# Kernel tuning notes

Measured on AMD Instinct MI355X. Metric: run time of the kernel, lower is better.

Reference implementation:

```python
import jax, jax.numpy as jnp
import numpy as np

ALPHA = 0.2  # LeakyReLU negative slope


def setup_inputs() -> dict:
    key = jax.random.key(0)
    k1, k2, k3, k4 = jax.random.split(key, 4)
    N, Fin, Fout = 8192, 256, 64
    inputs = {
        "input": jax.random.normal(k1, (N, Fin), dtype=jnp.float32),
        "adj": jax.random.randint(k2, (N, N), 0, 2, dtype=jnp.int32),
        "W": jax.random.normal(k3, (Fin, Fout), dtype=jnp.float32) * (1.414 * np.sqrt(2.0 / (Fin + Fout))),
        "a": jax.random.normal(k4, (2 * Fout, 1), dtype=jnp.float32) * (1.414 * np.sqrt(2.0 / (2 * Fout + 1))),
    }
    return inputs


def reference(input, adj, W, a):
    # h: [N, Fout]
    h = input @ W
    Fout = h.shape[1]
    # Decompose pairwise score: e[i,j] = leakyrelu(h[i]@a1 + h[j]@a2)
    # (mathematically identical to the original concat+matmul construction,
    #  but avoids the O(N^2 * 2F) intermediate)
    a1, a2 = a[:Fout, 0], a[Fout:, 0]
    s1 = h @ a1  # [N]
    s2 = h @ a2  # [N]
    e = jax.nn.leaky_relu(s1[:, None] + s2[None, :], negative_slope=ALPHA)  # [N, N]
    # Mask non-edges with -10 (as in the original), row softmax
    masked = jnp.where(adj > 0, e, jnp.float32(-10.0))
    attention = jax.nn.softmax(masked, axis=1)
    # dropout p=0.0 (eval/reference mode): identity
    h_prime = attention @ h  # [N, Fout]
    return jax.nn.elu(h_prime)  # concat=True path
```

## Files before the change

### kernel.cpp

```cpp
#include <hip/hip_runtime.h>
#include <hip/hip_bf16.h>
#include <cstdint>
#include <cstddef>

#define NN 8192
#define FIN 256
#define FOUT 64
#define ALPHA_SLOPE 0.2f
#define EXP_M10 4.5399929762484854e-05f

#define JSPLIT 2
#define STRIP 128
#define NSTRIP ((NN / JSPLIT) / STRIP)
#define WPITCH 272
#define HPITCH 272
#define CP 68

typedef short s16x8 __attribute__((ext_vector_type(8)));
typedef float f32x4 __attribute__((ext_vector_type(4)));
typedef int   i32x4 __attribute__((ext_vector_type(4)));

__device__ __forceinline__ unsigned short f2bf(float x) {
    union { float f; uint32_t u; } v; v.f = x;
    uint32_t u = v.u;
    return (unsigned short)((u + 0x7FFFu + ((u >> 16) & 1u)) >> 16);
}

__device__ __forceinline__ unsigned int pk2(float lo, float hi) {
    return (unsigned int)f2bf(lo) | ((unsigned int)f2bf(hi) << 16);
}

__global__ __launch_bounds__(256) void k_h(
    const float* __restrict__ input, const float* __restrict__ W,
    const float* __restrict__ a,
    unsigned short* __restrict__ htg, float* __restrict__ s1, float* __restrict__ s2)
{
    __shared__ __align__(16) unsigned short tile[64][28];
    const int wid  = threadIdx.x >> 6;
    const int lane = threadIdx.x & 63;
    const int i0   = blockIdx.x * 16;
    const int r0   = wid * 4;
    const float* inb = input + (size_t)(i0 + r0) * FIN;

    float acc0 = 0.f, acc1 = 0.f, acc2 = 0.f, acc3 = 0.f;
    #pragma unroll 4
    for (int c = 0; c < FIN; c += 4) {
        float w0 = W[(c + 0) * FOUT + lane];
        float w1 = W[(c + 1) * FOUT + lane];
        float w2 = W[(c + 2) * FOUT + lane];
        float w3 = W[(c + 3) * FOUT + lane];
        float4 x0 = *(const float4*)(inb + 0 * FIN + c);
        float4 x1 = *(const float4*)(inb + 1 * FIN + c);
        float4 x2 = *(const float4*)(inb + 2 * FIN + c);
        float4 x3 = *(const float4*)(inb + 3 * FIN + c);
        acc0 = fmaf(x0.x, w0, fmaf(x0.y, w1, fmaf(x0.z, w2, fmaf(x0.w, w3, acc0))));
        acc1 = fmaf(x1.x, w0, fmaf(x1.y, w1, fmaf(x1.z, w2, fmaf(x1.w, w3, acc1))));
        acc2 = fmaf(x2.x, w0, fmaf(x2.y, w1, fmaf(x2.z, w2, fmaf(x2.w, w3, acc2))));
        acc3 = fmaf(x3.x, w0, fmaf(x3.y, w1, fmaf(x3.z, w2, fmaf(x3.w, w3, acc3))));
    }

    const float a1v = a[lane], a2v = a[FOUT + lane];
    float accs[4] = {acc0, acc1, acc2, acc3};
    #pragma unroll
    for (int r = 0; r < 4; ++r) {
        float v1 = accs[r] * a1v;
        float v2 = accs[r] * a2v;
        #pragma unroll
        for (int off = 32; off; off >>= 1) {
            v1 += __shfl_xor(v1, off);
            v2 += __shfl_xor(v2, off);
        }
        if (lane == 0) { s1[i0 + r0 + r] = v1; s2[i0 + r0 + r] = v2; }
        tile[lane][r0 + r] = f2bf(accs[r]);
    }
    __syncthreads();

    const int feat = threadIdx.x >> 2;
    const int cg   = (threadIdx.x & 3) * 4;
    uint2 q = *(const uint2*)&tile[feat][cg];
    *(uint2*)(htg + (size_t)feat * NN + i0 + cg) = q;
}

__global__ __launch_bounds__(512, 4) void k_attn(
    const int* __restrict__ adj,
    const unsigned short* __restrict__ htg,
    const float* __restrict__ s1g, const float* __restrict__ s2g,
    float* __restrict__ slabs)
{
    __shared__ __align__(16) unsigned char wbuf[2][32 * WPITCH];
    __shared__ __align__(16) unsigned char hbuf[2][64 * HPITCH];

    const int t    = threadIdx.x;
    const int wid  = t >> 6;
    const int lane = t & 63;
    const int bi   = blockIdx.x >> 1;
    const int js   = blockIdx.x & 1;
    const int i0   = bi * 32;
    const int jbase = js * (NN / JSPLIT);
    const int m    = lane & 15;
    const int quad = lane >> 4;
    const int rg   = wid >> 2;
    const int kp   = (wid >> 1) & 1;
    const int fg   = wid & 1;

    const int srow  = t >> 4;
    const int scol  = (t & 15) * 8;
    const int sfeat = t >> 3;
    const int scol2 = (t & 7) * 16;
    const float s1v = s1g[i0 + srow];

    const short bd = (m == 0) ? (short)0x3F80 : (short)0;
    const s16x8 bden = {bd, bd, bd, bd, bd, bd, bd, bd};

    f32x4 accA = {0,0,0,0}, accB = {0,0,0,0}, accD = {0,0,0,0};

    const int* adjrow = adj + (size_t)(i0 + srow) * NN + jbase;
    const unsigned short* hrow = htg + (size_t)sfeat * NN + jbase;

    {
        i32x4  a0 = *(const i32x4*)(adjrow + scol);
        i32x4  a1 = *(const i32x4*)(adjrow + scol + 4);
        float4 v0 = *(const float4*)(s2g + jbase + scol);
        float4 v1 = *(const float4*)(s2g + jbase + scol + 4);
        s16x8  h0 = *(const s16x8*)(hrow + scol2);
        s16x8  h1 = *(const s16x8*)(hrow + scol2 + 8);

        float x0=s1v+v0.x, x1=s1v+v0.y, x2=s1v+v0.z, x3=s1v+v0.w;
        float x4=s1v+v1.x, x5=s1v+v1.y, x6=s1v+v1.z, x7=s1v+v1.w;
        float w0=(a0.x>0)?__expf(fmaxf(x0,ALPHA_SLOPE*x0)):EXP_M10;
        float w1=(a0.y>0)?__expf(fmaxf(x1,ALPHA_SLOPE*x1)):EXP_M10;
        float w2=(a0.z>0)?__expf(fmaxf(x2,ALPHA_SLOPE*x2)):EXP_M10;
        float w3=(a0.w>0)?__expf(fmaxf(x3,ALPHA_SLOPE*x3)):EXP_M10;
        float w4=(a1.x>0)?__expf(fmaxf(x4,ALPHA_SLOPE*x4)):EXP_M10;
        float w5=(a1.y>0)?__expf(fmaxf(x5,ALPHA_SLOPE*x5)):EXP_M10;
        float w6=(a1.z>0)?__expf(fmaxf(x6,ALPHA_SLOPE*x6)):EXP_M10;
        float w7=(a1.w>0)?__expf(fmaxf(x7,ALPHA_SLOPE*x7)):EXP_M10;
        uint4 pk = { pk2(w0,w1), pk2(w2,w3), pk2(w4,w5), pk2(w6,w7) };
        *(uint4*)&wbuf[0][srow * WPITCH + scol * 2] = pk;
        *(s16x8*)&hbuf[0][sfeat * HPITCH + scol2 * 2] = h0;
        *(s16x8*)&hbuf[0][sfeat * HPITCH + scol2 * 2 + 16] = h1;
    }
    __syncthreads();

    for (int s = 0; s < NSTRIP; ++s) {
        const int cur = s & 1, nxt = cur ^ 1;
        const bool more = (s + 1 < NSTRIP);

        i32x4 a0, a1; float4 v0, v1; s16x8 h0, h1;
        if (more) {
            const int j0n = (s + 1) * STRIP;
            a0 = *(const i32x4*)(adjrow + j0n + scol);
            a1 = *(const i32x4*)(adjrow + j0n + scol + 4);
            v0 = *(const float4*)(s2g + jbase + j0n + scol);
            v1 = *(const float4*)(s2g + jbase + j0n + scol + 4);
            h0 = *(const s16x8*)(hrow + j0n + scol2);
            h1 = *(const s16x8*)(hrow + j0n + scol2 + 8);
        }

        #pragma unroll
        for (int kq = 0; kq < 2; ++kq) {
            const int kk = kp * 2 + kq;
            const int cb = (kk * 32 + quad * 8) * 2;
            s16x8 af = *(const s16x8*)&wbuf[cur][(rg * 16 + m) * WPITCH + cb];
            const unsigned char* hb = &hbuf[cur][cb];
            if (fg == 0) {
                s16x8 b0 = *(const s16x8*)(hb + (m +  0) * HPITCH);
                s16x8 b1 = *(const s16x8*)(hb + (m + 16) * HPITCH);
                accA = __builtin_amdgcn_mfma_f32_16x16x32_bf16(af, b0, accA, 0, 0, 0);
                accB = __builtin_amdgcn_mfma_f32_16x16x32_bf16(af, b1, accB, 0, 0, 0);
            } else {
                s16x8 b2 = *(const s16x8*)(hb + (m + 32) * HPITCH);
                s16x8 b3 = *(const s16x8*)(hb + (m + 48) * HPITCH);
                accA = __builtin_amdgcn_mfma_f32_16x16x32_bf16(af, b2,   accA, 0, 0, 0);
                accB = __builtin_amdgcn_mfma_f32_16x16x32_bf16(af, b3,   accB, 0, 0, 0);
                accD = __builtin_amdgcn_mfma_f32_16x16x32_bf16(af, bden, accD, 0, 0, 0);
            }
        }

        if (more) {
            float x0=s1v+v0.x, x1=s1v+v0.y, x2=s1v+v0.z, x3=s1v+v0.w;
            float x4=s1v+v1.x, x5=s1v+v1.y, x6=s1v+v1.z, x7=s1v+v1.w;
            float w0=(a0.x>0)?__expf(fmaxf(x0,ALPHA_SLOPE*x0)):EXP_M10;
            float w1=(a0.y>0)?__expf(fmaxf(x1,ALPHA_SLOPE*x1)):EXP_M10;
            float w2=(a0.z>0)?__expf(fmaxf(x2,ALPHA_SLOPE*x2)):EXP_M10;
            float w3=(a0.w>0)?__expf(fmaxf(x3,ALPHA_SLOPE*x3)):EXP_M10;
            float w4=(a1.x>0)?__expf(fmaxf(x4,ALPHA_SLOPE*x4)):EXP_M10;
            float w5=(a1.y>0)?__expf(fmaxf(x5,ALPHA_SLOPE*x5)):EXP_M10;
            float w6=(a1.z>0)?__expf(fmaxf(x6,ALPHA_SLOPE*x6)):EXP_M10;
            float w7=(a1.w>0)?__expf(fmaxf(x7,ALPHA_SLOPE*x7)):EXP_M10;
            uint4 pk = { pk2(w0,w1), pk2(w2,w3), pk2(w4,w5), pk2(w6,w7) };
            *(uint4*)&wbuf[nxt][srow * WPITCH + scol * 2] = pk;
            *(s16x8*)&hbuf[nxt][sfeat * HPITCH + scol2 * 2] = h0;
            *(s16x8*)&hbuf[nxt][sfeat * HPITCH + scol2 * 2 + 16] = h1;
        }
        __syncthreads();
    }

    float* red = (float*)hbuf;
    float* myr = red + wid * (16 * 34);
    #pragma unroll
    for (int reg = 0; reg < 4; ++reg) {
        const int r = quad * 4 + reg;
        myr[r * 34 + m]      = accA[reg];
        myr[r * 34 + 16 + m] = accB[reg];
        if (fg == 1 && m == 0) myr[r * 34 + 32] = accD[reg];
    }
    __syncthreads();

    float* slab = slabs + (size_t)js * ((size_t)NN * CP);
    #pragma unroll
    for (int idx = t; idx < 32 * 64; idx += 512) {
        const int r = idx >> 6, c = idx & 63;
        const int rg2 = r >> 4, rr = r & 15;
        const int fg2 = c >> 5, lc = c & 31;
        float num = red[(rg2 * 4 + 0 + fg2) * 544 + rr * 34 + lc]
                  + red[(rg2 * 4 + 2 + fg2) * 544 + rr * 34 + lc];
        slab[(size_t)(i0 + r) * CP + c] = num;
        if (c == 0) {
            float den = red[(rg2 * 4 + 1) * 544 + rr * 34 + 32]
                      + red[(rg2 * 4 + 3) * 544 + rr * 34 + 32];
            slab[(size_t)(i0 + r) * CP + 64] = den;
        }
    }
}

__global__ __launch_bounds__(256) void k_norm(
    const float* __restrict__ slabs, float* __restrict__ out)
{
    int gid = blockIdx.x * 256 + threadIdx.x;
    int i = gid >> 6, k = gid & 63;
    float num = 0.f, den = 0.f;
    #pragma unroll
    for (int js = 0; js < JSPLIT; ++js) {
        const float* row = slabs + (size_t)js * ((size_t)NN * CP) + (size_t)i * CP;
        num += row[k];
        den += row[64];
    }
    float v = num / den;
    out[gid] = (v > 0.f) ? v : (__expf(v) - 1.f);
}

extern "C" void kernel_launch(void* const* d_in, const int* in_sizes, int n_in,
                              void* d_out, int out_size, void* d_ws, size_t ws_size,
                              hipStream_t stream) {
    const float* input = (const float*)d_in[0];
    const int*   adj   = (const int*)d_in[1];
    const float* W     = (const float*)d_in[2];
    const float* a     = (const float*)d_in[3];
    float* out = (float*)d_out;

    char* ws = (char*)d_ws;
    float* slabs = (float*)ws;
    size_t off = (size_t)JSPLIT * NN * CP * sizeof(float);
    unsigned short* htg = (unsigned short*)(ws + off);
    off += (size_t)FOUT * NN * sizeof(unsigned short);
    float* s1 = (float*)(ws + off); off += NN * sizeof(float);
    float* s2 = (float*)(ws + off);

    k_h   <<<NN / 16, 256, 0, stream>>>(input, W, a, htg, s1, s2);
    k_attn<<<(NN / 32) * JSPLIT, 512, 0, stream>>>(adj, htg, s1, s2, slabs);
    k_norm<<<NN * FOUT / 256, 256, 0, stream>>>(slabs, out);
}
```

Measured before the change: 390.7 us.

## Bit-pack adjacency and compute attention weights directly in MFMA registers

Adds a pre-pass that packs the int32 adjacency matrix into a bitmask with wave ballots. The attention kernel then reads mask bits instead of ints and builds the bf16 weight fragments in registers, with no LDS staging or barriers. It also folds log2(e) into s1/s2 so a raw v_exp_f32 can be used, uses the hardware pk bf16 convert, and splits the j dimension 8 ways for more blocks. The pack pass still reads the full adjacency matrix once, and the extra partial slabs raise reduction traffic in the normalise kernel.

Result: slower. 464.1 us (+18.8%).

```diff
diff --git a/kernel.cpp b/kernel.cpp
--- a/kernel.cpp
+++ b/kernel.cpp
@@ -8,12 +8,11 @@
 #define FOUT 64
 #define ALPHA_SLOPE 0.2f
 #define EXP_M10 4.5399929762484854e-05f
-
-#define JSPLIT 2
-#define STRIP 128
-#define NSTRIP ((NN / JSPLIT) / STRIP)
-#define WPITCH 272
-#define HPITCH 272
+#define LOG2E 1.4426950408889634f
+
+#define JC 8
+#define JSPAN (NN / JC)
+#define NSTRIP (JSPAN / 128)
 #define CP 68
 
 typedef short s16x8 __attribute__((ext_vector_type(8)));
@@ -26,8 +25,34 @@
     return (unsigned short)((u + 0x7FFFu + ((u >> 16) & 1u)) >> 16);
 }
 
-__device__ __forceinline__ unsigned int pk2(float lo, float hi) {
-    return (unsigned int)f2bf(lo) | ((unsigned int)f2bf(hi) << 16);
+__device__ __forceinline__ unsigned int cvtpk(float lo, float hi) {
+    unsigned int r;
+    asm("v_cvt_pk_bf16_f32 %0, %1, %2" : "=v"(r) : "v"(lo), "v"(hi));
+    return r;
+}
+
+__device__ __forceinline__ float fexp2(float x) {
+    float r;
+    asm("v_exp_f32 %0, %1" : "=v"(r) : "v"(x));
+    return r;
+}
+
+__global__ __launch_bounds__(256) void k_pack(
+    const int* __restrict__ adj, unsigned int* __restrict__ mask)
+{
+    const int total  = NN * NN;
+    const int stride = gridDim.x * 256;
+    int i = blockIdx.x * 256 + threadIdx.x;
+    for (; i < total; i += 2 * stride) {
+        int v0 = adj[i];
+        int v1 = adj[i + stride];
+        unsigned long long b0 = __ballot(v0 > 0);
+        unsigned long long b1 = __ballot(v1 > 0);
+        if ((threadIdx.x & 63) == 0) {
+            *(uint2*)&mask[i >> 5] = make_uint2((unsigned)b0, (unsigned)(b0 >> 32));
+            *(uint2*)&mask[(i + stride) >> 5] = make_uint2((unsigned)b1, (unsigned)(b1 >> 32));
+        }
+    }
 }
 
 __global__ __launch_bounds__(256) void k_h(
@@ -59,7 +84,7 @@
         acc3 = fmaf(x3.x, w0, fmaf(x3.y, w1, fmaf(x3.z, w2, fmaf(x3.w, w3, acc3))));
     }
 
-    const float a1v = a[lane], a2v = a[FOUT + lane];
+    const float a1v = a[lane] * LOG2E, a2v = a[FOUT + lane] * LOG2E;
     float accs[4] = {acc0, acc1, acc2, acc3};
     #pragma unroll
     for (int r = 0; r < 4; ++r) {
@@ -81,146 +106,101 @@
     *(uint2*)(htg + (size_t)feat * NN + i0 + cg) = q;
 }
 
-__global__ __launch_bounds__(512, 4) void k_attn(
-    const int* __restrict__ adj,
+__global__ __launch_bounds__(256, 4) void k_attn(
+    const unsigned int* __restrict__ mask,
     const unsigned short* __restrict__ htg,
     const float* __restrict__ s1g, const float* __restrict__ s2g,
     float* __restrict__ slabs)
 {
-    __shared__ __align__(16) unsigned char wbuf[2][32 * WPITCH];
-    __shared__ __align__(16) unsigned char hbuf[2][64 * HPITCH];
-
     const int t    = threadIdx.x;
-    const int wid  = t >> 6;
+    const int wb   = t >> 6;
     const int lane = t & 63;
-    const int bi   = blockIdx.x >> 1;
-    const int js   = blockIdx.x & 1;
-    const int i0   = bi * 32;
-    const int jbase = js * (NN / JSPLIT);
     const int m    = lane & 15;
     const int quad = lane >> 4;
-    const int rg   = wid >> 2;
-    const int kp   = (wid >> 1) & 1;
-    const int fg   = wid & 1;
-
-    const int srow  = t >> 4;
-    const int scol  = (t & 15) * 8;
-    const int sfeat = t >> 3;
-    const int scol2 = (t & 7) * 16;
-    const float s1v = s1g[i0 + srow];
+    const int jc   = blockIdx.x & (JC - 1);
+    const int rt   = (blockIdx.x >> 3) * 4 + wb;
+    const int row0 = rt * 16;
+    const int row  = row0 + m;
+    const int jbase = jc * JSPAN;
+
+    const float s1v = s1g[row];
+    const unsigned int*   mrow = mask + (size_t)row * (NN / 32) + (jbase >> 5);
+    const float*          s2b  = s2g + jbase + quad * 8;
+    const unsigned short* h0b  = htg + (size_t)(m +  0) * NN + jbase + quad * 8;
+    const unsigned short* h1b  = htg + (size_t)(m + 16) * NN + jbase + quad * 8;
+    const unsigned short* h2b  = htg + (size_t)(m + 32) * NN + jbase + quad * 8;
+    const unsigned short* h3b  = htg + (size_t)(m + 48) * NN + jbase + quad * 8;
 
     const short bd = (m == 0) ? (short)0x3F80 : (short)0;
     const s16x8 bden = {bd, bd, bd, bd, bd, bd, bd, bd};
 
-    f32x4 accA = {0,0,0,0}, accB = {0,0,0,0}, accD = {0,0,0,0};
-
-    const int* adjrow = adj + (size_t)(i0 + srow) * NN + jbase;
-    const unsigned short* hrow = htg + (size_t)sfeat * NN + jbase;
-
-    {
-        i32x4  a0 = *(const i32x4*)(adjrow + scol);
-        i32x4  a1 = *(const i32x4*)(adjrow + scol + 4);
-        float4 v0 = *(const float4*)(s2g + jbase + scol);
-        float4 v1 = *(const float4*)(s2g + jbase + scol + 4);
-        s16x8  h0 = *(const s16x8*)(hrow + scol2);
-        s16x8  h1 = *(const s16x8*)(hrow + scol2 + 8);
-
-        float x0=s1v+v0.x, x1=s1v+v0.y, x2=s1v+v0.z, x3=s1v+v0.w;
-        float x4=s1v+v1.x, x5=s1v+v1.y, x6=s1v+v1.z, x7=s1v+v1.w;
-        float w0=(a0.x>0)?__expf(fmaxf(x0,ALPHA_SLOPE*x0)):EXP_M10;
-        float w1=(a0.y>0)?__expf(fmaxf(x1,ALPHA_SLOPE*x1)):EXP_M10;
-        float w2=(a0.z>0)?__expf(fmaxf(x2,ALPHA_SLOPE*x2)):EXP_M10;
-        float w3=(a0.w>0)?__expf(fmaxf(x3,ALPHA_SLOPE*x3)):EXP_M10;
-        float w4=(a1.x>0)?__expf(fmaxf(x4,ALPHA_SLOPE*x4)):EXP_M10;
-        float w5=(a1.y>0)?__expf(fmaxf(x5,ALPHA_SLOPE*x5)):EXP_M10;
-        float w6=(a1.z>0)?__expf(fmaxf(x6,ALPHA_SLOPE*x6)):EXP_M10;
-        float w7=(a1.w>0)?__expf(fmaxf(x7,ALPHA_SLOPE*x7)):EXP_M10;
-        uint4 pk = { pk2(w0,w1), pk2(w2,w3), pk2(w4,w5), pk2(w6,w7) };
-        *(uint4*)&wbuf[0][srow * WPITCH + scol * 2] = pk;
-        *(s16x8*)&hbuf[0][sfeat * HPITCH + scol2 * 2] = h0;
-        *(s16x8*)&hbuf[0][sfeat * HPITCH + scol2 * 2 + 16] = h1;
-    }
-    __syncthreads();
+    f32x4 acc0 = {0,0,0,0}, acc1 = {0,0,0,0}, acc2 = {0,0,0,0}, acc3 = {0,0,0,0};
+    f32x4 accD = {0,0,0,0};
 
     for (int s = 0; s < NSTRIP; ++s) {
-        const int cur = s & 1, nxt = cur ^ 1;
-        const bool more = (s + 1 < NSTRIP);
-
-        i32x4 a0, a1; float4 v0, v1; s16x8 h0, h1;
-        if (more) {
-            const int j0n = (s + 1) * STRIP;
-            a0 = *(const i32x4*)(adjrow + j0n + scol);
-            a1 = *(const i32x4*)(adjrow + j0n + scol + 4);
-            v0 = *(const float4*)(s2g + jbase + j0n + scol);
-            v1 = *(const float4*)(s2g + jbase + j0n + scol + 4);
-            h0 = *(const s16x8*)(hrow + j0n + scol2);
-            h1 = *(const s16x8*)(hrow + j0n + scol2 + 8);
-        }
-
+        const int c0 = s * 128;
+        const i32x4 mw = *(const i32x4*)(mrow + (s << 2));
+
+        float4 sv[8];
         #pragma unroll
-        for (int kq = 0; kq < 2; ++kq) {
-            const int kk = kp * 2 + kq;
-            const int cb = (kk * 32 + quad * 8) * 2;
-            s16x8 af = *(const s16x8*)&wbuf[cur][(rg * 16 + m) * WPITCH + cb];
-            const unsigned char* hb = &hbuf[cur][cb];
-            if (fg == 0) {
-                s16x8 b0 = *(const s16x8*)(hb + (m +  0) * HPITCH);
-                s16x8 b1 = *(const s16x8*)(hb + (m + 16) * HPITCH);
-                accA = __builtin_amdgcn_mfma_f32_16x16x32_bf16(af, b0, accA, 0, 0, 0);
-                accB = __builtin_amdgcn_mfma_f32_16x16x32_bf16(af, b1, accB, 0, 0, 0);
-            } else {
-                s16x8 b2 = *(const s16x8*)(hb + (m + 32) * HPITCH);
-                s16x8 b3 = *(const s16x8*)(hb + (m + 48) * HPITCH);
-                accA = __builtin_amdgcn_mfma_f32_16x16x32_bf16(af, b2,   accA, 0, 0, 0);
-                accB = __builtin_amdgcn_mfma_f32_16x16x32_bf16(af, b3,   accB, 0, 0, 0);
-                accD = __builtin_amdgcn_mfma_f32_16x16x32_bf16(af, bden, accD, 0, 0, 0);
-            }
-        }
-
-        if (more) {
-            float x0=s1v+v0.x, x1=s1v+v0.y, x2=s1v+v0.z, x3=s1v+v0.w;
-            float x4=s1v+v1.x, x5=s1v+v1.y, x6=s1v+v1.z, x7=s1v+v1.w;
-            float w0=(a0.x>0)?__expf(fmaxf(x0,ALPHA_SLOPE*x0)):EXP_M10;
-            float w1=(a0.y>0)?__expf(fmaxf(x1,ALPHA_SLOPE*x1)):EXP_M10;
-            float w2=(a0.z>0)?__expf(fmaxf(x2,ALPHA_SLOPE*x2)):EXP_M10;
-            float w3=(a0.w>0)?__expf(fmaxf(x3,ALPHA_SLOPE*x3)):EXP_M10;
-            float w4=(a1.x>0)?__expf(fmaxf(x4,ALPHA_SLOPE*x4)):EXP_M10;
-            float w5=(a1.y>0)?__expf(fmaxf(x5,ALPHA_SLOPE*x5)):EXP_M10;
-            float w6=(a1.z>0)?__expf(fmaxf(x6,ALPHA_SLOPE*x6)):EXP_M10;
-            float w7=(a1.w>0)?__expf(fmaxf(x7,ALPHA_SLOPE*x7)):EXP_M10;
-            uint4 pk = { pk2(w0,w1), pk2(w2,w3), pk2(w4,w5), pk2(w6,w7) };
-            *(uint4*)&wbuf[nxt][srow * WPITCH + scol * 2] = pk;
-            *(s16x8*)&hbuf[nxt][sfeat * HPITCH + scol2 * 2] = h0;
-            *(s16x8*)&hbuf[nxt][sfeat * HPITCH + scol2 * 2 + 16] = h1;
-        }
-        __syncthreads();
-    }
-
-    float* red = (float*)hbuf;
-    float* myr = red + wid * (16 * 34);
+        for (int q = 0; q < 4; ++q) {
+            sv[2*q]   = *(const float4*)(s2b + c0 + q * 32);
+            sv[2*q+1] = *(const float4*)(s2b + c0 + q * 32 + 4);
+        }
+
+        #pragma unroll
+        for (int kk = 0; kk < 4; ++kk) {
+            const unsigned int mb = ((unsigned int)mw[kk]) >> (quad * 8);
+            const float4 va = sv[2*kk], vb = sv[2*kk+1];
+
+            float y0 = s1v + va.x, y1 = s1v + va.y, y2 = s1v + va.z, y3 = s1v + va.w;
+            float y4 = s1v + vb.x, y5 = s1v + vb.y, y6 = s1v + vb.z, y7 = s1v + vb.w;
+            float e0 = fexp2(fmaxf(y0, ALPHA_SLOPE * y0));
+            float e1 = fexp2(fmaxf(y1, ALPHA_SLOPE * y1));
+            float e2 = fexp2(fmaxf(y2, ALPHA_SLOPE * y2));
+            float e3 = fexp2(fmaxf(y3, ALPHA_SLOPE * y3));
+            float e4 = fexp2(fmaxf(y4, ALPHA_SLOPE * y4));
+            float e5 = fexp2(fmaxf(y5, ALPHA_SLOPE * y5));
+            float e6 = fexp2(fmaxf(y6, ALPHA_SLOPE * y6));
+            float e7 = fexp2(fmaxf(y7, ALPHA_SLOPE * y7));
+            float w0 = (mb &   1u) ? e0 : EXP_M10;
+            float w1 = (mb &   2u) ? e1 : EXP_M10;
+            float w2 = (mb &   4u) ? e2 : EXP_M10;
+            float w3 = (mb &   8u) ? e3 : EXP_M10;
+            float w4 = (mb &  16u) ? e4 : EXP_M10;
+            float w5 = (mb &  32u) ? e5 : EXP_M10;
+            float w6 = (mb &  64u) ? e6 : EXP_M10;
+            float w7 = (mb & 128u) ? e7 : EXP_M10;
+
+            union { unsigned int u[4]; s16x8 v; } af;
+            af.u[0] = cvtpk(w0, w1);
+            af.u[1] = cvtpk(w2, w3);
+            af.u[2] = cvtpk(w4, w5);
+            af.u[3] = cvtpk(w6, w7);
+
+            const int cc = c0 + kk * 32;
+            s16x8 b0 = *(const s16x8*)(h0b + cc);
+            s16x8 b1 = *(const s16x8*)(h1b + cc);
+            s16x8 b2 = *(const s16x8*)(h2b + cc);
+            s16x8 b3 = *(const s16x8*)(h3b + cc);
+
+            acc0 = __builtin_amdgcn_mfma_f32_16x16x32_bf16(af.v, b0,   acc0, 0, 0, 0);
+            acc1 = __builtin_amdgcn_mfma_f32_16x16x32_bf16(af.v, b1,   acc1, 0, 0, 0);
+            acc2 = __builtin_amdgcn_mfma_f32_16x16x32_bf16(af.v, b2,   acc2, 0, 0, 0);
+            acc3 = __builtin_amdgcn_mfma_f32_16x16x32_bf16(af.v, b3,   acc3, 0, 0, 0);
+            accD = __builtin_amdgcn_mfma_f32_16x16x32_bf16(af.v, bden, accD, 0, 0, 0);
+        }
+    }
+
+    float* slab = slabs + (size_t)jc * ((size_t)NN * CP) + (size_t)row0 * CP;
     #pragma unroll
-    for (int reg = 0; reg < 4; ++reg) {
-        const int r = quad * 4 + reg;
-        myr[r * 34 + m]      = accA[reg];
-        myr[r * 34 + 16 + m] = accB[reg];
-        if (fg == 1 && m == 0) myr[r * 34 + 32] = accD[reg];
-    }
-    __syncthreads();
-
-    float* slab = slabs + (size_t)js * ((size_t)NN * CP);
-    #pragma unroll
-    for (int idx = t; idx < 32 * 64; idx += 512) {
-        const int r = idx >> 6, c = idx & 63;
-        const int rg2 = r >> 4, rr = r & 15;
-        const int fg2 = c >> 5, lc = c & 31;
-        float num = red[(rg2 * 4 + 0 + fg2) * 544 + rr * 34 + lc]
-                  + red[(rg2 * 4 + 2 + fg2) * 544 + rr * 34 + lc];
-        slab[(size_t)(i0 + r) * CP + c] = num;
-        if (c == 0) {
-            float den = red[(rg2 * 4 + 1) * 544 + rr * 34 + 32]
-                      + red[(rg2 * 4 + 3) * 544 + rr * 34 + 32];
-            slab[(size_t)(i0 + r) * CP + 64] = den;
-        }
+    for (int r = 0; r < 4; ++r) {
+        const int ro = quad * 4 + r;
+        slab[ro * CP +  0 + m] = acc0[r];
+        slab[ro * CP + 16 + m] = acc1[r];
+        slab[ro * CP + 32 + m] = acc2[r];
+        slab[ro * CP + 48 + m] = acc3[r];
+        if (m == 0) slab[ro * CP + 64] = accD[r];
     }
 }
 
@@ -231,10 +211,10 @@
     int i = gid >> 6, k = gid & 63;
     float num = 0.f, den = 0.f;
     #pragma unroll
-    for (int js = 0; js < JSPLIT; ++js) {
-        const float* row = slabs + (size_t)js * ((size_t)NN * CP) + (size_t)i * CP;
-        num += row[k];
-        den += row[64];
+    for (int jc = 0; jc < JC; ++jc) {
+        const float* rowp = slabs + (size_t)jc * ((size_t)NN * CP) + (size_t)i * CP;
+        num += rowp[k];
+        den += rowp[64];
     }
     float v = num / den;
     out[gid] = (v > 0.f) ? v : (__expf(v) - 1.f);
@@ -251,13 +231,15 @@
 
     char* ws = (char*)d_ws;
     float* slabs = (float*)ws;
-    size_t off = (size_t)JSPLIT * NN * CP * sizeof(float);
+    size_t off = (size_t)JC * NN * CP * sizeof(float);
     unsigned short* htg = (unsigned short*)(ws + off);
     off += (size_t)FOUT * NN * sizeof(unsigned short);
     float* s1 = (float*)(ws + off); off += NN * sizeof(float);
-    float* s2 = (float*)(ws + off);
-
+    float* s2 = (float*)(ws + off); off += NN * sizeof(float);
+    unsigned int* mask = (unsigned int*)(ws + off);
+
+    k_pack<<<2048, 256, 0, stream>>>(adj, mask);
     k_h   <<<NN / 16, 256, 0, stream>>>(input, W, a, htg, s1, s2);
-    k_attn<<<(NN / 32) * JSPLIT, 512, 0, stream>>>(adj, htg, s1, s2, slabs);
+    k_attn<<<(NN / 16 / 4) * JC, 256, 0, stream>>>(mask, htg, s1, s2, slabs);
     k_norm<<<NN * FOUT / 256, 256, 0, stream>>>(slabs, out);
 }
```
